# Optimization experiments

Measured on AMD Instinct MI355X. Metric: run time of the kernel, lower is better.

## Reference

```python
import jax, jax.numpy as jnp
import numpy as np

TAU = 2.0
THR = 1.0
ALPHA = 10.0
FLOW_SCALE = 16.0  # 2 ** flow_scale_pow2 (=4)
DECAY = 1.0 - 1.0 / TAU


def conv2d(x, w, b=None, stride=1, pad=0):
    # x: [N,C,H,W], w: [O,I,kh,kw]
    out = jax.lax.conv_general_dilated(
        x, w, (stride, stride), [(pad, pad), (pad, pad)],
        dimension_numbers=('NCHW', 'OIHW', 'NCHW'))
    if b is not None:
        out = out + b[None, :, None, None]
    return out


@jax.custom_vjp
def spike(v):
    return (v > 0).astype(v.dtype)

def _spike_fwd(v):
    return (v > 0).astype(v.dtype), v

def _spike_bwd(v, g):
    s = jax.nn.sigmoid(ALPHA * v)
    return (g * ALPHA * s * (1.0 - s),)

spike.defvjp(_spike_fwd, _spike_bwd)


def lif(x, w, b, mem, stride, pad):
    """Conv + leaky-integrate-fire with soft reset. mem init 0 -> first step mem=cur."""
    cur = conv2d(x, w, b, stride, pad)
    mem = mem * DECAY + cur
    s = spike(mem - THR)
    mem = mem - s * THR
    return s, mem


def up2(x):
    return jnp.repeat(jnp.repeat(x, 2, axis=2), 2, axis=3)


def forward(x, w_e1, b_e1, w_e2, b_e2, w_e3, b_e3, w_d3, b_d3,
            w_d2, b_d2, w_d1, b_d1, w_skip2, w_skip1, w_flow, b_flow):
    N, T, C, H, W = x.shape
    bc = w_e1.shape[0]  # base_ch = 32
    z = lambda c, h, w: jnp.zeros((N, c, h, w), x.dtype)
    init = (
        z(bc, H // 2, W // 2),      # mem_e1
        z(2 * bc, H // 4, W // 4),  # mem_e2
        z(4 * bc, H // 8, W // 8),  # mem_e3
        z(2 * bc, H // 4, W // 4),  # mem_d3
        z(bc, H // 2, W // 2),      # mem_d2
        z(bc, H, W),                # mem_d1
        z(bc, H // 2, W // 2),      # mean_e1 (zeros + /(t+1) rule == None-init)
        z(2 * bc, H // 4, W // 4),  # mean_e2
        z(2, H, W),                 # flow_mean
    )

    def step(carry, inp):
        t, xt = inp
        m1, m2, m3, md3, md2, md1, me1, me2, fm = carry
        s1, m1 = lif(xt, w_e1, b_e1, m1, 2, 2)
        s2, m2 = lif(s1, w_e2, b_e2, m2, 2, 1)
        s3, m3 = lif(s2, w_e3, b_e3, m3, 2, 1)
        tf = (t + 1).astype(xt.dtype)
        me1 = me1 + (s1 - me1) / tf
        me2 = me2 + (s2 - me2) / tf
        d3, md3 = lif(up2(s3), w_d3, b_d3, md3, 1, 1)
        d3 = d3 + conv2d(me2, w_skip2)
        d2, md2 = lif(up2(d3), w_d2, b_d2, md2, 1, 1)
        d2 = d2 + conv2d(me1, w_skip1)
        d1, md1 = lif(up2(d2), w_d1, b_d1, md1, 1, 1)
        flow = conv2d(d1, w_flow, b_flow, 1, 1) * FLOW_SCALE
        fm = fm + (flow - fm) / tf
        return (m1, m2, m3, md3, md2, md1, me1, me2, fm), flow

    _, flows = jax.lax.scan(step, init, (jnp.arange(T), jnp.moveaxis(x, 1, 0)))
    return flows[-1]  # return_last_flow=True -> flow of final timestep [N,2,H,W]


def setup_inputs() -> dict:
    key = jax.random.key(0)
    ks = jax.random.split(key, 16)
    N, T, H, W, bc = 4, 8, 256, 256, 32

    def w(k, o, i, kh, kw):
        return jax.random.normal(k, (o, i, kh, kw), jnp.float32) / np.sqrt(i * kh * kw)

    return {
        'x': jax.random.uniform(ks[0], (N, T, 2, H, W), jnp.float32),
        'w_e1': w(ks[1], bc, 2, 5, 5), 'b_e1': jnp.zeros((bc,), jnp.float32),
        'w_e2': w(ks[2], 2 * bc, bc, 3, 3), 'b_e2': jnp.zeros((2 * bc,), jnp.float32),
        'w_e3': w(ks[3], 4 * bc, 2 * bc, 3, 3), 'b_e3': jnp.zeros((4 * bc,), jnp.float32),
        'w_d3': w(ks[4], 2 * bc, 4 * bc, 3, 3), 'b_d3': jnp.zeros((2 * bc,), jnp.float32),
        'w_d2': w(ks[5], bc, 2 * bc, 3, 3), 'b_d2': jnp.zeros((bc,), jnp.float32),
        'w_d1': w(ks[6], bc, bc, 3, 3), 'b_d1': jnp.zeros((bc,), jnp.float32),
        'w_skip2': w(ks[7], 2 * bc, 2 * bc, 1, 1),
        'w_skip1': w(ks[8], bc, bc, 1, 1),
        'w_flow': w(ks[9], 2, bc, 3, 3), 'b_flow': jnp.zeros((2,), jnp.float32),
    }


def reference(x, w_e1, b_e1, w_e2, b_e2, w_e3, b_e3, w_d3, b_d3,
              w_d2, b_d2, w_d1, b_d1, w_skip2, w_skip1, w_flow, b_flow):
    return forward(x, w_e1, b_e1, w_e2, b_e2, w_e3, b_e3, w_d3, b_d3,
                   w_d2, b_d2, w_d1, b_d1, w_skip2, w_skip1, w_flow, b_flow)
```

## Files before the change

### kernel.cpp

```cpp
#include <hip/hip_runtime.h>
#include <cstdint>
#include <cstddef>


static constexpr float THRc   = 1.0f;
static constexpr float DECAYc = 0.5f;

__global__ __launch_bounds__(256) void prep_collapse(const float* __restrict__ w,
                                                     float* __restrict__ wc, int pairs)
{
    int idx = blockIdx.x * 256 + threadIdx.x;
    if (idx >= pairs) return;
    float a[3][3];
#pragma unroll
    for (int i = 0; i < 3; ++i)
#pragma unroll
        for (int j = 0; j < 3; ++j) a[i][j] = w[idx * 9 + i * 3 + j];
    float rs[2][2][3];
#pragma unroll
    for (int kx = 0; kx < 3; ++kx) {
        rs[0][0][kx] = a[0][kx];
        rs[0][1][kx] = a[1][kx] + a[2][kx];
        rs[1][0][kx] = a[0][kx] + a[1][kx];
        rs[1][1][kx] = a[2][kx];
    }
#pragma unroll
    for (int py = 0; py < 2; ++py)
#pragma unroll
        for (int px = 0; px < 2; ++px)
#pragma unroll
            for (int r = 0; r < 2; ++r) {
                float c0, c1;
                if (px == 0) { c0 = rs[py][r][0];               c1 = rs[py][r][1] + rs[py][r][2]; }
                else         { c0 = rs[py][r][0] + rs[py][r][1]; c1 = rs[py][r][2]; }
                wc[idx * 16 + ((py * 2 + px) * 2 + r) * 2 + 0] = c0;
                wc[idx * 16 + ((py * 2 + px) * 2 + r) * 2 + 1] = c1;
            }
}

template<int IC, int ICC, int OC, int SIH, int SIW, int CPT, int YPB, int OCT,
         int NW, int SKIP_IC, int SKC>
__global__ __launch_bounds__(NW * 64) void dec_conv(
    const float* __restrict__ in,
    const float* __restrict__ wc,
    const float* __restrict__ bias,
    float* __restrict__ mem,
    float* __restrict__ out,
    const float* __restrict__ skip_in,
    const float* __restrict__ skip_w)
{
    constexpr int NT   = NW * 64;
    constexpr int LPT  = SIW / CPT;
    static_assert(LPT * YPB == 64, "wave must tile the band");
    static_assert((ICC & (ICC - 1)) == 0, "ICC pow2");
    static_assert((CPT & 1) == 0, "CPT even for b64 reads");
    constexpr int OC_B = NW * OCT;
    constexpr int NOCB = OC / OC_B;
    constexpr int NYB  = SIH / YPB;
    constexpr int SP   = SIW + 8;
    constexpr int SR   = YPB + 2;
    constexpr int OH   = 2 * SIH, OW = 2 * SIW;
    constexpr int NCH  = IC / ICC;
    constexpr int W4   = SIW / 4;
    constexpr int TILE = ICC * SR * SP;
    constexpr int WTSZ = OC_B * ICC * 16;
    constexpr int OROWS = 2 * YPB;
    constexpr int SKTILE = (SKIP_IC > 0) ? SKC * OROWS * OW : 0;
    constexpr int BASE = TILE > SKTILE ? TILE : SKTILE;
    constexpr int NR2  = CPT / 2 + 2;
    constexpr int NV   = (2 * CPT) / 4;

    __shared__ __align__(16) float smem[BASE + WTSZ];
    float* const sb = smem;
    float* const wt = smem + BASE;

    int b = blockIdx.x;
    const int ocb = b % NOCB; b /= NOCB;
    const int yb  = b % NYB;  b /= NYB;
    const int n   = b;
    const int y0  = yb * YPB;

    const int lane = threadIdx.x & 63;
    const int wav  = threadIdx.x >> 6;
    const int cl   = lane % LPT;
    const int yp   = lane / LPT;
    const int c0   = cl * CPT;
    const int y    = y0 + yp;

    const int oc0 = __builtin_amdgcn_readfirstlane(ocb * OC_B + wav * OCT);

    for (int f = threadIdx.x; f < ICC * SR * 2; f += NT) {
        int side = f & 1;
        int t    = f >> 1;
        int r    = t % SR;
        int ic   = t / SR;
        sb[(ic * SR + r) * SP + (side ? (SIW + 4) : 3)] = 0.0f;
    }

    float acc[OCT][2][2 * CPT];
#pragma unroll
    for (int j = 0; j < OCT; ++j) {
        float bv = bias[oc0 + j];
#pragma unroll
        for (int py = 0; py < 2; ++py)
#pragma unroll
            for (int q = 0; q < 2 * CPT; ++q) acc[j][py][q] = bv;
    }

    const float* inn = in + (size_t)n * IC * SIH * SIW;

    for (int ch = 0; ch < NCH; ++ch) {
        __syncthreads();
        const float* inb = inn + (size_t)ch * ICC * SIH * SIW;
        constexpr int SLOTS = ICC * SR * W4;
        for (int f = threadIdx.x; f < SLOTS; f += NT) {
            int c4 = f & (W4 - 1);
            int t  = f / W4;
            int r  = t % SR;
            int ic = t / SR;
            int sy = y0 - 1 + r;
            float4 v = make_float4(0.f, 0.f, 0.f, 0.f);
            if (sy >= 0 && sy < SIH)
                v = *reinterpret_cast<const float4*>(
                        inb + (size_t)ic * SIH * SIW + (size_t)sy * SIW + 4 * c4);
            *reinterpret_cast<float4*>(&sb[(ic * SR + r) * SP + 4 + 4 * c4]) = v;
        }
        for (int f = threadIdx.x; f < WTSZ / 4; f += NT) {
            int j   = f / (ICC * 4);
            int rem = f & (ICC * 4 - 1);
            int ic  = rem >> 2;
            int k4  = rem & 3;
            *reinterpret_cast<float4*>(&wt[f * 4]) =
                *reinterpret_cast<const float4*>(
                    wc + ((size_t)(ocb * OC_B + j) * IC + ch * ICC + ic) * 16 + 4 * k4);
        }
        __syncthreads();
        for (int ic = 0; ic < ICC; ++ic) {
            float s[3][CPT + 2];
#pragma unroll
            for (int r = 0; r < 3; ++r) {
                float2 t2[NR2];
#pragma unroll
                for (int i = 0; i < NR2; ++i)
                    t2[i] = *reinterpret_cast<const float2*>(
                        &sb[(ic * SR + yp + r) * SP + c0 + 2 + 2 * i]);
#pragma unroll
                for (int k = 0; k < CPT + 2; ++k) {
                    constexpr int dummy = 0; (void)dummy;
                    int p = k + 1;
                    s[r][k] = (p & 1) ? t2[p >> 1].y : t2[p >> 1].x;
                }
            }
#pragma unroll
            for (int j = 0; j < OCT; ++j) {
                const float* wl = wt + ((wav * OCT + j) * ICC + ic) * 16;
                float4 w0 = *reinterpret_cast<const float4*>(wl + 0);
                float4 w1 = *reinterpret_cast<const float4*>(wl + 4);
                float4 w2 = *reinterpret_cast<const float4*>(wl + 8);
                float4 w3 = *reinterpret_cast<const float4*>(wl + 12);
                const float wv[16] = {w0.x, w0.y, w0.z, w0.w, w1.x, w1.y, w1.z, w1.w,
                                      w2.x, w2.y, w2.z, w2.w, w3.x, w3.y, w3.z, w3.w};
#pragma unroll
                for (int py = 0; py < 2; ++py)
#pragma unroll
                    for (int cc = 0; cc < CPT; ++cc)
#pragma unroll
                        for (int px = 0; px < 2; ++px) {
                            float v = acc[j][py][cc * 2 + px];
#pragma unroll
                            for (int rr = 0; rr < 2; ++rr)
#pragma unroll
                                for (int c2 = 0; c2 < 2; ++c2)
                                    v += wv[(py * 2 + px) * 4 + rr * 2 + c2]
                                       * s[py + rr][cc + px + c2];
                            acc[j][py][cc * 2 + px] = v;
                        }
            }
        }
    }

    float sk[OCT][2][2 * CPT] = {};
    if constexpr (SKIP_IC > 0) {
        constexpr int NSK = SKIP_IC / SKC;
        constexpr int OW4 = OW / 4;
        const float* skn = skip_in + (size_t)n * SKIP_IC * OH * OW;
        for (int sc = 0; sc < NSK; ++sc) {
            __syncthreads();
            for (int f = threadIdx.x; f < SKC * OROWS * OW4; f += NT) {
                int c4 = f & (OW4 - 1);
                int t  = f / OW4;
                int r  = t & (OROWS - 1);
                int ic = t / OROWS;
                *reinterpret_cast<float4*>(&sb[(ic * OROWS + r) * OW + 4 * c4]) =
                    *reinterpret_cast<const float4*>(
                        skn + ((size_t)(sc * SKC + ic) * OH + 2 * y0 + r) * OW + 4 * c4);
            }
            __syncthreads();
            float wsk[OCT][SKC];
#pragma unroll
            for (int j = 0; j < OCT; ++j)
#pragma unroll
                for (int ic = 0; ic < SKC; ++ic)
                    wsk[j][ic] = skip_w[(size_t)(oc0 + j) * SKIP_IC + sc * SKC + ic];
#pragma unroll
            for (int ic = 0; ic < SKC; ++ic)
#pragma unroll
                for (int py = 0; py < 2; ++py)
#pragma unroll
                    for (int v = 0; v < NV; ++v) {
                        float4 sv = *reinterpret_cast<const float4*>(
                            &sb[(ic * OROWS + 2 * yp + py) * OW + 2 * c0 + 4 * v]);
#pragma unroll
                        for (int j = 0; j < OCT; ++j) {
                            sk[j][py][4 * v + 0] += wsk[j][ic] * sv.x;
                            sk[j][py][4 * v + 1] += wsk[j][ic] * sv.y;
                            sk[j][py][4 * v + 2] += wsk[j][ic] * sv.z;
                            sk[j][py][4 * v + 3] += wsk[j][ic] * sv.w;
                        }
                    }
        }
    }

    const bool wout = (out != nullptr);
#pragma unroll
    for (int j = 0; j < OCT; ++j)
#pragma unroll
        for (int py = 0; py < 2; ++py) {
            size_t ob = (((size_t)n * OC + oc0 + j) * OH + (2 * y + py)) * OW + 2 * c0;
#pragma unroll
            for (int v = 0; v < NV; ++v) {
                float4 mv = *reinterpret_cast<const float4*>(&mem[ob + 4 * v]);
                float4 ov, nm;
                float m0 = mv.x * DECAYc + acc[j][py][4 * v + 0];
                float m1 = mv.y * DECAYc + acc[j][py][4 * v + 1];
                float m2 = mv.z * DECAYc + acc[j][py][4 * v + 2];
                float m3 = mv.w * DECAYc + acc[j][py][4 * v + 3];
                float s0 = (m0 - THRc) > 0.0f ? 1.0f : 0.0f;
                float s1 = (m1 - THRc) > 0.0f ? 1.0f : 0.0f;
                float s2 = (m2 - THRc) > 0.0f ? 1.0f : 0.0f;
                float s3 = (m3 - THRc) > 0.0f ? 1.0f : 0.0f;
                nm.x = m0 - s0 * THRc; nm.y = m1 - s1 * THRc;
                nm.z = m2 - s2 * THRc; nm.w = m3 - s3 * THRc;
                *reinterpret_cast<float4*>(&mem[ob + 4 * v]) = nm;
                if (wout) {
                    ov.x = s0 + sk[j][py][4 * v + 0];
                    ov.y = s1 + sk[j][py][4 * v + 1];
                    ov.z = s2 + sk[j][py][4 * v + 2];
                    ov.w = s3 + sk[j][py][4 * v + 3];
                    *reinterpret_cast<float4*>(&out[ob + 4 * v]) = ov;
                }
            }
        }
}

template<int IC, int ICC, int OC, int IH, int IW, int K, int CPT, int LPT, int OCT, bool DO_MEAN>
__global__ __launch_bounds__(256) void enc_conv(
    const float* __restrict__ in, int in_nstride,
    const float* __restrict__ wgt,
    const float* __restrict__ bias,
    float* __restrict__ mem,
    float* __restrict__ out,
    float* __restrict__ mean,
    float inv_tf)
{
    constexpr int P    = K / 2;
    constexpr int OH   = IH / 2, OW = IW / 2;
    constexpr int SPr  = 4 + IW + P;
    constexpr int SP   = (SPr + 3) & ~3;
    constexpr int OC_B = 4 * OCT;
    constexpr int NOCB = OC / OC_B;
    constexpr int RL   = 2 * CPT + 2 * P - 1;
    constexpr int NCH  = IC / ICC;
    constexpr int W4   = IW / 4;
    static_assert(LPT * CPT == OW, "lanes x CPT must cover OW");
    static_assert((ICC & (ICC - 1)) == 0, "ICC pow2");

    __shared__ float sb[K][ICC][SP];

    int b = blockIdx.x;
    const int ocb = b % NOCB; b /= NOCB;
    const int y   = b % OH;   b /= OH;
    const int n   = b;

    const int lane = threadIdx.x & 63;
    const int wav  = threadIdx.x >> 6;
    const int x0   = (lane % LPT) * CPT;
    const int oc0  = __builtin_amdgcn_readfirstlane(ocb * OC_B + wav * OCT);

    for (int f = threadIdx.x; f < K * ICC * 2 * P; f += 256) {
        int h  = f % (2 * P);
        int t  = f / (2 * P);
        int ic = t & (ICC - 1);
        int r  = t / ICC;
        int col = (h < P) ? (4 - P + h) : (4 + IW + h - P);
        sb[r][ic][col] = 0.0f;
    }

    float acc[OCT][CPT];
#pragma unroll
    for (int j = 0; j < OCT; ++j) {
        float bv = bias[oc0 + j];
#pragma unroll
        for (int cc = 0; cc < CPT; ++cc) acc[j][cc] = bv;
    }

    const float* inn = in + (size_t)n * (size_t)in_nstride;

    for (int ch = 0; ch < NCH; ++ch) {
        __syncthreads();
        const float* inb = inn + (size_t)ch * ICC * IH * IW;
        constexpr int SLOTS = K * ICC * W4;
        for (int f = threadIdx.x; f < SLOTS; f += 256) {
            int c4 = f & (W4 - 1);
            int t  = f / W4;
            int ic = t & (ICC - 1);
            int r  = t / ICC;
            int sy = 2 * y - P + r;
            float4 v = make_float4(0.f, 0.f, 0.f, 0.f);
            if (sy >= 0 && sy < IH)
                v = *reinterpret_cast<const float4*>(
                        inb + (size_t)ic * IH * IW + (size_t)sy * IW + 4 * c4);
            *reinterpret_cast<float4*>(&sb[r][ic][4 + 4 * c4]) = v;
        }
        __syncthreads();
        for (int ic = 0; ic < ICC; ++ic) {
            float s[K][RL];
#pragma unroll
            for (int r = 0; r < K; ++r)
#pragma unroll
                for (int k = 0; k < RL; ++k)
                    s[r][k] = sb[r][ic][4 - P + 2 * x0 + k];
            const float* wp = wgt + ((size_t)oc0 * IC + ch * ICC + ic) * (K * K);
#pragma unroll
            for (int j = 0; j < OCT; ++j) {
                float wv[K * K];
#pragma unroll
                for (int k = 0; k < K * K; ++k) wv[k] = wp[(size_t)j * IC * K * K + k];
#pragma unroll
                for (int cc = 0; cc < CPT; ++cc)
#pragma unroll
                    for (int ky = 0; ky < K; ++ky)
#pragma unroll
                        for (int kx = 0; kx < K; ++kx)
                            acc[j][cc] += wv[ky * K + kx] * s[ky][2 * cc + kx];
            }
        }
    }

    if (lane < LPT) {
#pragma unroll
        for (int j = 0; j < OCT; ++j) {
            size_t ob = (((size_t)n * OC + oc0 + j) * OH + y) * OW + x0;
#pragma unroll
            for (int cc = 0; cc < CPT; ++cc) {
                float m  = mem[ob + cc] * DECAYc + acc[j][cc];
                float sp = (m - THRc) > 0.0f ? 1.0f : 0.0f;
                mem[ob + cc] = m - sp * THRc;
                if constexpr (DO_MEAN) {
                    float mv = mean[ob + cc];
                    mean[ob + cc] = mv + (sp - mv) * inv_tf;
                }
                out[ob + cc] = sp;
            }
        }
    }
}

template<int IC, int OC, int IH, int IW, int OH, int OW,
         int K, int STRIDE, int PAD, bool UP2, int SKIP_IC,
         bool DO_LIF, bool DO_MEAN>
__global__ __launch_bounds__(256) void conv_fused(
    const float* __restrict__ in, int in_nstride,
    const float* __restrict__ wgt,
    const float* __restrict__ bias,
    float* __restrict__ mem,
    float* __restrict__ out,
    const float* __restrict__ skip_in,
    const float* __restrict__ skip_w,
    float* __restrict__ mean,
    float inv_tf, float outscale)
{
    constexpr int VEC  = 4;
    constexpr int OWV  = OW / VEC;
    constexpr int WSZ  = IC * K * K;
    constexpr int SIH  = UP2 ? IH / 2 : IH;
    constexpr int SIW  = UP2 ? IW / 2 : IW;
    constexpr int RLEN = (VEC - 1) * STRIDE + K;

    __shared__ float sw[WSZ];

    const int bstart = blockIdx.x * 256;
    const int oc = (bstart / (OH * OWV)) % OC;

    for (int i = threadIdx.x; i < WSZ; i += 256) sw[i] = wgt[oc * WSZ + i];
    __syncthreads();

    const int idx = bstart + threadIdx.x;
    const int wx  = idx % OWV;
    int tt        = idx / OWV;
    const int oy  = tt % OH; tt /= OH;
    tt /= OC;
    const int n   = tt;
    const int ox0 = wx * VEC;

    const float bv = bias ? bias[oc] : 0.0f;
    float acc[VEC];
#pragma unroll
    for (int v = 0; v < VEC; ++v) acc[v] = bv;

    const float* inn = in + (size_t)n * (size_t)in_nstride;

    for (int ic = 0; ic < IC; ++ic) {
        const float* inc = inn + (size_t)ic * (SIH * SIW);
#pragma unroll
        for (int ky = 0; ky < K; ++ky) {
            const int uy = oy * STRIDE + ky - PAD;
            const bool rowok = (uy >= 0) & (uy < IH);
            int sy = UP2 ? (uy >> 1) : uy;
            sy = sy < 0 ? 0 : (sy > SIH - 1 ? SIH - 1 : sy);
            const float* __restrict__ row = inc + (size_t)sy * SIW;

            float r[RLEN];
#pragma unroll
            for (int j = 0; j < RLEN; ++j) {
                const int ux = ox0 * STRIDE - PAD + j;
                const bool ok = rowok & (ux >= 0) & (ux < IW);
                int sx = UP2 ? (ux >> 1) : ux;
                sx = sx < 0 ? 0 : (sx > SIW - 1 ? SIW - 1 : sx);
                r[j] = ok ? row[sx] : 0.0f;
            }
#pragma unroll
            for (int kx = 0; kx < K; ++kx) {
                const float wv = sw[(ic * K + ky) * K + kx];
#pragma unroll
                for (int v = 0; v < VEC; ++v)
                    acc[v] += r[v * STRIDE + kx] * wv;
            }
        }
    }

    const size_t obase = ((((size_t)n * OC + oc) * OH) + oy) * (size_t)OW + ox0;
#pragma unroll
    for (int v = 0; v < VEC; ++v) out[obase + v] = acc[v] * outscale;
}

extern "C" void kernel_launch(void* const* d_in, const int* in_sizes, int n_in,
                              void* d_out, int out_size, void* d_ws, size_t ws_size,
                              hipStream_t stream)
{
    const float* x     = (const float*)d_in[0];
    const float* w_e1  = (const float*)d_in[1];
    const float* b_e1  = (const float*)d_in[2];
    const float* w_e2  = (const float*)d_in[3];
    const float* b_e2  = (const float*)d_in[4];
    const float* w_e3  = (const float*)d_in[5];
    const float* b_e3  = (const float*)d_in[6];
    const float* w_d3  = (const float*)d_in[7];
    const float* b_d3  = (const float*)d_in[8];
    const float* w_d2  = (const float*)d_in[9];
    const float* b_d2  = (const float*)d_in[10];
    const float* w_d1  = (const float*)d_in[11];
    const float* b_d1  = (const float*)d_in[12];
    const float* w_sk2 = (const float*)d_in[13];
    const float* w_sk1 = (const float*)d_in[14];
    const float* w_fl  = (const float*)d_in[15];
    const float* b_fl  = (const float*)d_in[16];
    float* outp = (float*)d_out;

    float* ws = (float*)d_ws;
    size_t off = 0;
    auto alloc = [&](size_t nelem) { float* p = ws + off; off += nelem; return p; };

    float* m1  = alloc(4UL * 32 * 128 * 128);
    float* m2  = alloc(4UL * 64 * 64 * 64);
    float* m3  = alloc(4UL * 128 * 32 * 32);
    float* md3 = alloc(4UL * 64 * 64 * 64);
    float* md2 = alloc(4UL * 32 * 128 * 128);
    float* md1 = alloc(4UL * 32 * 256 * 256);
    float* me1 = alloc(4UL * 32 * 128 * 128);
    float* me2 = alloc(4UL * 64 * 64 * 64);
    const size_t zcount = off;
    float* s1  = alloc(4UL * 32 * 128 * 128);
    float* s2  = alloc(4UL * 64 * 64 * 64);
    float* s3  = alloc(4UL * 128 * 32 * 32);
    float* d3a = alloc(4UL * 64 * 64 * 64);
    float* d2a = alloc(4UL * 32 * 128 * 128);
    float* d1a = alloc(4UL * 32 * 256 * 256);
    float* wc3 = alloc(64UL * 128 * 16);
    float* wc2 = alloc(32UL * 64 * 16);
    float* wc1 = alloc(32UL * 32 * 16);
    (void)ws_size; (void)in_sizes; (void)n_in; (void)out_size;

    hipMemsetAsync(d_ws, 0, zcount * sizeof(float), stream);

    prep_collapse<<<(64 * 128 + 255) / 256, 256, 0, stream>>>(w_d3, wc3, 64 * 128);
    prep_collapse<<<(32 * 64 + 255) / 256, 256, 0, stream>>>(w_d2, wc2, 32 * 64);
    prep_collapse<<<(32 * 32 + 255) / 256, 256, 0, stream>>>(w_d1, wc1, 32 * 32);

    for (int t = 0; t < 8; ++t) {
        const float inv_tf = 1.0f / (float)(t + 1);
        const float* xt = x + (size_t)t * 2 * 256 * 256;

        enc_conv<2, 2, 32, 256, 256, 5, 2, 64, 2, true>
            <<<4 * 128 * 4, 256, 0, stream>>>(xt, 8 * 2 * 256 * 256, w_e1, b_e1,
                                              m1, s1, me1, inv_tf);
        enc_conv<32, 16, 64, 128, 128, 3, 1, 64, 2, true>
            <<<4 * 64 * 8, 256, 0, stream>>>(s1, 32 * 128 * 128, w_e2, b_e2,
                                             m2, s2, me2, inv_tf);
        enc_conv<64, 32, 128, 64, 64, 3, 1, 32, 4, false>
            <<<4 * 32 * 8, 256, 0, stream>>>(s2, 64 * 64 * 64, w_e3, b_e3,
                                             m3, s3, nullptr, inv_tf);
        dec_conv<128, 32, 64, 32, 32, 2, 4, 2, 1, 64, 8>
            <<<1024, 64, 0, stream>>>(s3, wc3, b_d3, md3, d3a, me2, w_sk2);
        dec_conv<64, 16, 32, 64, 64, 2, 2, 2, 4, 32, 8>
            <<<512, 256, 0, stream>>>(d3a, wc2, b_d2, md2, d2a, me1, w_sk1);
        dec_conv<32, 8, 32, 128, 128, 4, 2, 4, 4, 0, 1>
            <<<512, 256, 0, stream>>>(d2a, wc1, b_d1, md1,
                                      (t == 7) ? d1a : nullptr, nullptr, nullptr);
        if (t == 7) {
            conv_fused<32, 2, 256, 256, 256, 256, 3, 1, 1, false, 0, false, false>
                <<<512, 256, 0, stream>>>(d1a, 32 * 256 * 256, w_fl, b_fl,
                                          nullptr, outp, nullptr, nullptr, nullptr, inv_tf, 16.0f);
        }
    }
}
```

Measured before the change: 2.389 ms.

## Load decoder conv weights directly to registers with ping-pong prefetch, retile launches

The decoder transposed-conv kernel stops staging collapsed weights in shared memory. Each wave now loads its weights from global memory into registers, using an lzero trick so the loads are issued as vector rather than scalar loads, and double-buffers them (wA/wB) one input channel ahead. The input window reads are simplified to a fixed CPT=2 pattern. All three decoder launches are retiled (OCT, YPB, CPT, wave count, grid size), and the weight buffers are padded so the one-past-the-end prefetch stays in bounds. This removes the LDS weight traffic and one sync dependency, at the cost of more register pressure and per-lane redundant global weight loads.

```diff
diff --git a/kernel.cpp b/kernel.cpp
--- a/kernel.cpp
+++ b/kernel.cpp
@@ -5,6 +5,15 @@
 
 static constexpr float THRc   = 1.0f;
 static constexpr float DECAYc = 0.5f;
+
+__device__ __forceinline__ float getc(const float4& v, int k) {
+    switch (k & 3) {
+        case 0: return v.x;
+        case 1: return v.y;
+        case 2: return v.z;
+        default: return v.w;
+    }
+}
 
 __global__ __launch_bounds__(256) void prep_collapse(const float* __restrict__ w,
                                                      float* __restrict__ wc, int pairs)
@@ -51,9 +60,9 @@
 {
     constexpr int NT   = NW * 64;
     constexpr int LPT  = SIW / CPT;
+    static_assert(CPT == 2, "template written for CPT=2");
     static_assert(LPT * YPB == 64, "wave must tile the band");
-    static_assert((ICC & (ICC - 1)) == 0, "ICC pow2");
-    static_assert((CPT & 1) == 0, "CPT even for b64 reads");
+    static_assert((ICC & 1) == 0, "ICC even for wA/wB ping-pong");
     constexpr int OC_B = NW * OCT;
     constexpr int NOCB = OC / OC_B;
     constexpr int NYB  = SIH / YPB;
@@ -63,16 +72,11 @@
     constexpr int NCH  = IC / ICC;
     constexpr int W4   = SIW / 4;
     constexpr int TILE = ICC * SR * SP;
-    constexpr int WTSZ = OC_B * ICC * 16;
     constexpr int OROWS = 2 * YPB;
     constexpr int SKTILE = (SKIP_IC > 0) ? SKC * OROWS * OW : 0;
     constexpr int BASE = TILE > SKTILE ? TILE : SKTILE;
-    constexpr int NR2  = CPT / 2 + 2;
-    constexpr int NV   = (2 * CPT) / 4;
-
-    __shared__ __align__(16) float smem[BASE + WTSZ];
-    float* const sb = smem;
-    float* const wt = smem + BASE;
+
+    __shared__ __align__(16) float sb[BASE];
 
     int b = blockIdx.x;
     const int ocb = b % NOCB; b /= NOCB;
@@ -89,6 +93,11 @@
 
     const int oc0 = __builtin_amdgcn_readfirstlane(ocb * OC_B + wav * OCT);
 
+    int lzero;
+    asm volatile("v_mov_b32 %0, 0" : "=v"(lzero));
+    const float4* wlane = reinterpret_cast<const float4*>(wc) + lzero;
+    const int wbase = oc0 * IC * 4;
+
     for (int f = threadIdx.x; f < ICC * SR * 2; f += NT) {
         int side = f & 1;
         int t    = f >> 1;
@@ -109,6 +118,46 @@
 
     const float* inn = in + (size_t)n * IC * SIH * SIW;
 
+    float4 wA[OCT * 4], wB[OCT * 4];
+    auto wload = [&](int icg, float4* dst) {
+#pragma unroll
+        for (int j = 0; j < OCT; ++j)
+#pragma unroll
+            for (int g = 0; g < 4; ++g)
+                dst[j * 4 + g] = wlane[wbase + (j * IC + icg) * 4 + g];
+    };
+
+    auto compute = [&](int icl, const float4* w) {
+        float s[3][4];
+#pragma unroll
+        for (int r = 0; r < 3; ++r) {
+            const int rb  = (icl * SR + yp + r) * SP;
+            const int hb  = rb + 3 + c0;
+            float2 own = *reinterpret_cast<const float2*>(&sb[rb + 4 + c0]);
+            float sl = sb[hb];
+            float sr = sb[hb + 3];
+            s[r][0] = sl; s[r][1] = own.x; s[r][2] = own.y; s[r][3] = sr;
+        }
+#pragma unroll
+        for (int j = 0; j < OCT; ++j)
+#pragma unroll
+            for (int py = 0; py < 2; ++py)
+#pragma unroll
+                for (int cc = 0; cc < CPT; ++cc)
+#pragma unroll
+                    for (int px = 0; px < 2; ++px) {
+                        float v = acc[j][py][cc * 2 + px];
+#pragma unroll
+                        for (int rr = 0; rr < 2; ++rr)
+#pragma unroll
+                            for (int c2 = 0; c2 < 2; ++c2)
+                                v += getc(w[j * 4 + py * 2 + px], rr * 2 + c2)
+                                   * s[py + rr][cc + px + c2];
+                        acc[j][py][cc * 2 + px] = v;
+                    }
+    };
+
+    wload(0, wA);
     for (int ch = 0; ch < NCH; ++ch) {
         __syncthreads();
         const float* inb = inn + (size_t)ch * ICC * SIH * SIW;
@@ -125,60 +174,17 @@
                         inb + (size_t)ic * SIH * SIW + (size_t)sy * SIW + 4 * c4);
             *reinterpret_cast<float4*>(&sb[(ic * SR + r) * SP + 4 + 4 * c4]) = v;
         }
-        for (int f = threadIdx.x; f < WTSZ / 4; f += NT) {
-            int j   = f / (ICC * 4);
-            int rem = f & (ICC * 4 - 1);
-            int ic  = rem >> 2;
-            int k4  = rem & 3;
-            *reinterpret_cast<float4*>(&wt[f * 4]) =
-                *reinterpret_cast<const float4*>(
-                    wc + ((size_t)(ocb * OC_B + j) * IC + ch * ICC + ic) * 16 + 4 * k4);
-        }
         __syncthreads();
-        for (int ic = 0; ic < ICC; ++ic) {
-            float s[3][CPT + 2];
-#pragma unroll
-            for (int r = 0; r < 3; ++r) {
-                float2 t2[NR2];
-#pragma unroll
-                for (int i = 0; i < NR2; ++i)
-                    t2[i] = *reinterpret_cast<const float2*>(
-                        &sb[(ic * SR + yp + r) * SP + c0 + 2 + 2 * i]);
-#pragma unroll
-                for (int k = 0; k < CPT + 2; ++k) {
-                    constexpr int dummy = 0; (void)dummy;
-                    int p = k + 1;
-                    s[r][k] = (p & 1) ? t2[p >> 1].y : t2[p >> 1].x;
-                }
-            }
-#pragma unroll
-            for (int j = 0; j < OCT; ++j) {
-                const float* wl = wt + ((wav * OCT + j) * ICC + ic) * 16;
-                float4 w0 = *reinterpret_cast<const float4*>(wl + 0);
-                float4 w1 = *reinterpret_cast<const float4*>(wl + 4);
-                float4 w2 = *reinterpret_cast<const float4*>(wl + 8);
-                float4 w3 = *reinterpret_cast<const float4*>(wl + 12);
-                const float wv[16] = {w0.x, w0.y, w0.z, w0.w, w1.x, w1.y, w1.z, w1.w,
-                                      w2.x, w2.y, w2.z, w2.w, w3.x, w3.y, w3.z, w3.w};
-#pragma unroll
-                for (int py = 0; py < 2; ++py)
-#pragma unroll
-                    for (int cc = 0; cc < CPT; ++cc)
-#pragma unroll
-                        for (int px = 0; px < 2; ++px) {
-                            float v = acc[j][py][cc * 2 + px];
-#pragma unroll
-                            for (int rr = 0; rr < 2; ++rr)
-#pragma unroll
-                                for (int c2 = 0; c2 < 2; ++c2)
-                                    v += wv[(py * 2 + px) * 4 + rr * 2 + c2]
-                                       * s[py + rr][cc + px + c2];
-                            acc[j][py][cc * 2 + px] = v;
-                        }
-            }
-        }
-    }
-
+        const int icg0 = ch * ICC;
+        for (int ic = 0; ic < ICC; ic += 2) {
+            wload(icg0 + ic + 1, wB);
+            compute(ic, wA);
+            wload(icg0 + ic + 2, wA);
+            compute(ic + 1, wB);
+        }
+    }
+
+    constexpr int NV = (2 * CPT) / 4;
     float sk[OCT][2][2 * CPT] = {};
     if constexpr (SKIP_IC > 0) {
         constexpr int NSK = SKIP_IC / SKC;
@@ -189,7 +195,7 @@
             for (int f = threadIdx.x; f < SKC * OROWS * OW4; f += NT) {
                 int c4 = f & (OW4 - 1);
                 int t  = f / OW4;
-                int r  = t & (OROWS - 1);
+                int r  = t % OROWS;
                 int ic = t / OROWS;
                 *reinterpret_cast<float4*>(&sb[(ic * OROWS + r) * OW + 4 * c4]) =
                     *reinterpret_cast<const float4*>(
@@ -486,9 +492,9 @@
     float* d3a = alloc(4UL * 64 * 64 * 64);
     float* d2a = alloc(4UL * 32 * 128 * 128);
     float* d1a = alloc(4UL * 32 * 256 * 256);
-    float* wc3 = alloc(64UL * 128 * 16);
-    float* wc2 = alloc(32UL * 64 * 16);
-    float* wc1 = alloc(32UL * 32 * 16);
+    float* wc3 = alloc(64UL * 128 * 16 + 64);
+    float* wc2 = alloc(32UL * 64 * 16 + 64);
+    float* wc1 = alloc(32UL * 32 * 16 + 64);
     (void)ws_size; (void)in_sizes; (void)n_in; (void)out_size;
 
     hipMemsetAsync(d_ws, 0, zcount * sizeof(float), stream);
@@ -510,13 +516,13 @@
         enc_conv<64, 32, 128, 64, 64, 3, 1, 32, 4, false>
             <<<4 * 32 * 8, 256, 0, stream>>>(s2, 64 * 64 * 64, w_e3, b_e3,
                                              m3, s3, nullptr, inv_tf);
-        dec_conv<128, 32, 64, 32, 32, 2, 4, 2, 1, 64, 8>
-            <<<1024, 64, 0, stream>>>(s3, wc3, b_d3, md3, d3a, me2, w_sk2);
+        dec_conv<128, 32, 64, 32, 32, 2, 4, 1, 4, 64, 8>
+            <<<4 * 8 * 16, 256, 0, stream>>>(s3, wc3, b_d3, md3, d3a, me2, w_sk2);
         dec_conv<64, 16, 32, 64, 64, 2, 2, 2, 4, 32, 8>
-            <<<512, 256, 0, stream>>>(d3a, wc2, b_d2, md2, d2a, me1, w_sk1);
-        dec_conv<32, 8, 32, 128, 128, 4, 2, 4, 4, 0, 1>
-            <<<512, 256, 0, stream>>>(d2a, wc1, b_d1, md1,
-                                      (t == 7) ? d1a : nullptr, nullptr, nullptr);
+            <<<4 * 32 * 4, 256, 0, stream>>>(d3a, wc2, b_d2, md2, d2a, me1, w_sk1);
+        dec_conv<32, 8, 32, 128, 128, 2, 1, 2, 4, 0, 1>
+            <<<4 * 128 * 4, 256, 0, stream>>>(d2a, wc1, b_d1, md1,
+                                              (t == 7) ? d1a : nullptr, nullptr, nullptr);
         if (t == 7) {
             conv_fused<32, 2, 256, 256, 256, 256, 3, 1, 1, false, 0, false, false>
                 <<<512, 256, 0, stream>>>(d1a, 32 * 256 * 256, w_fl, b_fl,
```

After: 2.222 ms. -7.0%, faster.
